# Performance work log

Measured on AMD Instinct MI355X. Metric: run time of the kernel, lower is better.

Reference implementation:

```python
import jax, jax.numpy as jnp
import numpy as np

ALPHA = -10.0  # softmax sharpness on |x - bin| distances
TAU = 0.0
TAU2 = 0.0
EPS = 1e-10

B, F, L, K = 32, 64, 1024, 32


def setup_inputs() -> dict:
    key = jax.random.key(0)
    k1, k2 = jax.random.split(key)
    x = jax.random.normal(k1, (B, F, L), dtype=jnp.float32)
    bins = jax.random.normal(k2, (K,), dtype=jnp.float32)
    return {"x": x, "bins": bins}


def reference(x, bins):
    # dist: [B, F, L, K] = |x[..., None] - bins|
    dist = jnp.abs(x[..., None] - bins)
    # soft assignment over the K bins (training path of the module)
    soft = jax.nn.softmax(ALPHA * dist, axis=-1)
    assignment = soft + EPS

    # weighted quantization loss: sum of per-bin mean of sqrt(assignment)
    quant = jnp.sum(jnp.mean(jnp.sqrt(assignment), axis=(0, 1, 2)))
    weighted_quant_loss = jnp.stack([quant, jnp.float32(TAU2)])[None, :]  # [1, 2]

    # code entropy of average assignment distribution
    p = jnp.mean(assignment, axis=(0, 1, 2))  # [K]
    code_entropy = -jnp.sum(p * jnp.log(p))
    weighted_code_entropy = jnp.stack([code_entropy, jnp.float32(TAU)])[None, :]  # [1, 2]

    # soft reconstruction against the bins: [B, F, L]
    bit_code = jnp.einsum('bflk,k->bfl', assignment, bins)
    return bit_code, weighted_code_entropy, weighted_quant_loss
```

## Files before the change

### kernel.cpp

```cpp
#include <hip/hip_runtime.h>

#define K      32
#define KH     16
#define TPB    256
#define NB     2048
#define EPT    8
#define NTOT   (32 * 64 * 1024)
#define PSTRIDE (NB * (TPB / 2))

__device__ __forceinline__ float wave_reduce_sum(float v) {
#pragma unroll
  for (int m = 1; m < 64; m <<= 1) v += __shfl_xor(v, m, 64);
  return v;
}

__device__ __forceinline__ float pair_lane_reduce(float v) {
#pragma unroll
  for (int m = 2; m < 64; m <<= 1) v += __shfl_xor(v, m, 64);
  return v;
}

__global__ __launch_bounds__(TPB)
void ssq_main(const float* __restrict__ x, const float* __restrict__ bins,
              float* __restrict__ out, float* __restrict__ partials) {
  const int tid  = threadIdx.x;
  const int half = tid & 1;
  const int pslot = blockIdx.x * (TPB / 2) + (tid >> 1);

  float binv[KH];
#pragma unroll
  for (int j = 0; j < KH; ++j) binv[j] = bins[KH * half + j];
  float bs_local = 0.f;
#pragma unroll
  for (int j = 0; j < KH; ++j) bs_local += binv[j];
  const float binsum = bs_local + __shfl_xor(bs_local, 1, 64);
  const float epsb = 1e-10f * binsum;

  float xs[EPT];
#pragma unroll
  for (int e = 0; e < EPT; ++e) xs[e] = x[pslot + e * PSTRIDE];

  float sAcc[KH];
#pragma unroll
  for (int j = 0; j < KH; ++j) sAcc[j] = 0.f;
  float q = 0.f;

  const float Ch = -7.213475204444817f;

#pragma unroll 1
  for (int e = 0; e < EPT; ++e) {
    const float xv = xs[e];
    float t[KH];
    float s0 = 0.f, s1 = 0.f, h0 = 0.f, h1 = 0.f, b0 = 0.f, b1 = 0.f;
#pragma unroll
    for (int j = 0; j < KH; j += 2) {
      float ha = __builtin_amdgcn_exp2f(Ch * fabsf(xv - binv[j + 0]));
      float hb = __builtin_amdgcn_exp2f(Ch * fabsf(xv - binv[j + 1]));
      float ta = ha * ha, tb = hb * hb;
      t[j + 0] = ta; t[j + 1] = tb;
      s0 += ta; s1 += tb;
      h0 += ha; h1 += hb;
      b0 = fmaf(ta, binv[j + 0], b0);
      b1 = fmaf(tb, binv[j + 1], b1);
    }
    const float s_loc = s0 + s1;
    const float b_loc = b0 + b1;
    const float s_full = s_loc + __shfl_xor(s_loc, 1, 64);
    const float b_full = b_loc + __shfl_xor(b_loc, 1, 64);
    const float inv = __builtin_amdgcn_rcpf(s_full);
    q = fmaf(h0 + h1, __builtin_amdgcn_rsqf(s_full), q);
    if (half == 0) out[pslot + e * PSTRIDE] = fmaf(b_full, inv, epsb);
#pragma unroll
    for (int j = 0; j < KH; ++j) sAcc[j] = fmaf(t[j], inv, sAcc[j]);
  }

  __shared__ float red[4][K + 1];
  const int lane = tid & 63, wv = tid >> 6;
#pragma unroll
  for (int j = 0; j < KH; ++j) {
    float v = pair_lane_reduce(sAcc[j]);
    if (lane < 2) red[wv][KH * lane + j] = v;
  }
  {
    float v = wave_reduce_sum(q);
    if (lane == 0) red[wv][K] = v;
  }
  __syncthreads();
  if (tid < K + 1) {
    float v = red[0][tid] + red[1][tid] + red[2][tid] + red[3][tid];
    partials[tid * NB + blockIdx.x] = v;
  }
}

__global__ __launch_bounds__(TPB)
void ssq_reduce(const float* __restrict__ partials, float* __restrict__ sums) {
  const float* p = partials + blockIdx.x * NB;
  const int tid  = threadIdx.x;
  float s = 0.f;
#pragma unroll
  for (int j = 0; j < NB / TPB; ++j) s += p[tid + j * TPB];
  s = wave_reduce_sum(s);
  __shared__ float red[4];
  if ((tid & 63) == 0) red[tid >> 6] = s;
  __syncthreads();
  if (tid == 0) sums[blockIdx.x] = red[0] + red[1] + red[2] + red[3];
}

__global__ void ssq_final(const float* __restrict__ sums, float* __restrict__ out) {
  const int lane = threadIdx.x;
  float e = 0.f;
  if (lane < K) {
    float p = sums[lane] * (1.0f / (float)NTOT) + 1e-10f;
    e = -p * __logf(p);
  }
  e = wave_reduce_sum(e);
  if (lane == 0) {
    out[NTOT + 0] = e;
    out[NTOT + 1] = 0.f;
    out[NTOT + 2] = sums[K] * (1.0f / (float)NTOT);
    out[NTOT + 3] = 0.f;
  }
}

extern "C" void kernel_launch(void* const* d_in, const int* in_sizes, int n_in,
                              void* d_out, int out_size, void* d_ws, size_t ws_size,
                              hipStream_t stream) {
  const float* x    = (const float*)d_in[0];
  const float* bins = (const float*)d_in[1];
  float* out        = (float*)d_out;
  float* partials   = (float*)d_ws;
  float* sums       = partials + (K + 1) * NB;

  ssq_main  <<<NB,    TPB, 0, stream>>>(x, bins, out, partials);
  ssq_reduce<<<K + 1, TPB, 0, stream>>>(partials, sums);
  ssq_final <<<1,     64,  0, stream>>>(sums, out);
}
```

Baseline: 83.97 us.

## Replace per-bin softmax loop with sorted-bin prefix sums and binary search

Sorts the bins in a prep kernel and precomputes prefix and suffix sums of exp(±c·bin), so each element's softmax denominator, reconstruction and sqrt sums need only a binary search plus a few exponentials, not 32. Per-bin assignment mass is gathered with shared-memory atomics into two split-point accumulators and rebuilt in a merged tail kernel. This removes most of the exp work, but exp(±14.4·x) factorisation can overflow or lose precision for large |x| or bins, and shared atomics may contend.

```diff
diff --git a/kernel.cpp b/kernel.cpp
--- a/kernel.cpp
+++ b/kernel.cpp
@@ -1,12 +1,11 @@
 #include <hip/hip_runtime.h>
 
 #define K      32
-#define KH     16
 #define TPB    256
 #define NB     2048
-#define EPT    8
 #define NTOT   (32 * 64 * 1024)
-#define PSTRIDE (NB * (TPB / 2))
+#define CL2    14.4269504088896341f
+#define TFLOATS 232
 
 __device__ __forceinline__ float wave_reduce_sum(float v) {
 #pragma unroll
@@ -14,111 +13,142 @@
   return v;
 }
 
-__device__ __forceinline__ float pair_lane_reduce(float v) {
+
+__global__ void ssq_prep(const float* __restrict__ bins, float* __restrict__ tg) {
+  const int lane = threadIdx.x;
+  float bv = (lane < K) ? bins[lane] : 0.f;
+  int rank = 0;
 #pragma unroll
-  for (int m = 2; m < 64; m <<= 1) v += __shfl_xor(v, m, 64);
-  return v;
-}
-
-__global__ __launch_bounds__(TPB)
-void ssq_main(const float* __restrict__ x, const float* __restrict__ bins,
-              float* __restrict__ out, float* __restrict__ partials) {
-  const int tid  = threadIdx.x;
-  const int half = tid & 1;
-  const int pslot = blockIdx.x * (TPB / 2) + (tid >> 1);
-
-  float binv[KH];
-#pragma unroll
-  for (int j = 0; j < KH; ++j) binv[j] = bins[KH * half + j];
-  float bs_local = 0.f;
-#pragma unroll
-  for (int j = 0; j < KH; ++j) bs_local += binv[j];
-  const float binsum = bs_local + __shfl_xor(bs_local, 1, 64);
-  const float epsb = 1e-10f * binsum;
-
-  float xs[EPT];
-#pragma unroll
-  for (int e = 0; e < EPT; ++e) xs[e] = x[pslot + e * PSTRIDE];
-
-  float sAcc[KH];
-#pragma unroll
-  for (int j = 0; j < KH; ++j) sAcc[j] = 0.f;
-  float q = 0.f;
-
-  const float Ch = -7.213475204444817f;
-
-#pragma unroll 1
-  for (int e = 0; e < EPT; ++e) {
-    const float xv = xs[e];
-    float t[KH];
-    float s0 = 0.f, s1 = 0.f, h0 = 0.f, h1 = 0.f, b0 = 0.f, b1 = 0.f;
-#pragma unroll
-    for (int j = 0; j < KH; j += 2) {
-      float ha = __builtin_amdgcn_exp2f(Ch * fabsf(xv - binv[j + 0]));
-      float hb = __builtin_amdgcn_exp2f(Ch * fabsf(xv - binv[j + 1]));
-      float ta = ha * ha, tb = hb * hb;
-      t[j + 0] = ta; t[j + 1] = tb;
-      s0 += ta; s1 += tb;
-      h0 += ha; h1 += hb;
-      b0 = fmaf(ta, binv[j + 0], b0);
-      b1 = fmaf(tb, binv[j + 1], b1);
+  for (int j = 0; j < K; ++j) {
+    float bj = __shfl(bv, j, 64);
+    rank += (bj < bv) || (bj == bv && j < lane);
+  }
+  __shared__ float sb[K];
+  if (lane < K) sb[rank] = bv;
+  __syncthreads();
+  if (lane <= K) {
+    float A = 0.f, B = 0.f, Ab = 0.f, Bb = 0.f, Ah = 0.f, Bh = 0.f;
+    for (int k = 0; k < K; ++k) {
+      float s   = sb[k];
+      float e   = __builtin_amdgcn_exp2f( CL2 * s);
+      float em  = __builtin_amdgcn_exp2f(-CL2 * s);
+      float eh  = __builtin_amdgcn_exp2f( 0.5f * CL2 * s);
+      float ehm = __builtin_amdgcn_exp2f(-0.5f * CL2 * s);
+      if (k < lane) { A += e;  Ab = fmaf(s, e,  Ab); Ah += eh;  }
+      else          { B += em; Bb = fmaf(s, em, Bb); Bh += ehm; }
     }
-    const float s_loc = s0 + s1;
-    const float b_loc = b0 + b1;
-    const float s_full = s_loc + __shfl_xor(s_loc, 1, 64);
-    const float b_full = b_loc + __shfl_xor(b_loc, 1, 64);
-    const float inv = __builtin_amdgcn_rcpf(s_full);
-    q = fmaf(h0 + h1, __builtin_amdgcn_rsqf(s_full), q);
-    if (half == 0) out[pslot + e * PSTRIDE] = fmaf(b_full, inv, epsb);
-#pragma unroll
-    for (int j = 0; j < KH; ++j) sAcc[j] = fmaf(t[j], inv, sAcc[j]);
+    tg[ 33 + lane] = A;  tg[ 66 + lane] = B;
+    tg[ 99 + lane] = Ab; tg[132 + lane] = Bb;
+    tg[165 + lane] = Ah; tg[198 + lane] = Bh;
   }
-
-  __shared__ float red[4][K + 1];
-  const int lane = tid & 63, wv = tid >> 6;
-#pragma unroll
-  for (int j = 0; j < KH; ++j) {
-    float v = pair_lane_reduce(sAcc[j]);
-    if (lane < 2) red[wv][KH * lane + j] = v;
-  }
-  {
-    float v = wave_reduce_sum(q);
-    if (lane == 0) red[wv][K] = v;
-  }
-  __syncthreads();
-  if (tid < K + 1) {
-    float v = red[0][tid] + red[1][tid] + red[2][tid] + red[3][tid];
-    partials[tid * NB + blockIdx.x] = v;
+  if (lane < K) tg[lane] = sb[lane];
+  if (lane == 0) {
+    tg[K] = 0.f;
+    float bs = 0.f;
+    for (int k = 0; k < K; ++k) bs += sb[k];
+    tg[231] = 1e-10f * bs;
   }
 }
 
-__global__ __launch_bounds__(TPB)
-void ssq_reduce(const float* __restrict__ partials, float* __restrict__ sums) {
-  const float* p = partials + blockIdx.x * NB;
-  const int tid  = threadIdx.x;
-  float s = 0.f;
-#pragma unroll
-  for (int j = 0; j < NB / TPB; ++j) s += p[tid + j * TPB];
-  s = wave_reduce_sum(s);
-  __shared__ float red[4];
-  if ((tid & 63) == 0) red[tid >> 6] = s;
-  __syncthreads();
-  if (tid == 0) sums[blockIdx.x] = red[0] + red[1] + red[2] + red[3];
+__device__ __forceinline__ void ssq_elem(float xv, const float* __restrict__ Tf,
+                                         float* __restrict__ bU,
+                                         float* __restrict__ bV,
+                                         float epsb, float& q, float& bit) {
+  const float* sb = Tf;
+  int b_ = 0;
+  b_ += (sb[b_ + 15] <= xv) ? 16 : 0;
+  b_ += (sb[b_ +  7] <= xv) ?  8 : 0;
+  b_ += (sb[b_ +  3] <= xv) ?  4 : 0;
+  b_ += (sb[b_ +  1] <= xv) ?  2 : 0;
+  b_ += (sb[b_]      <= xv) ?  1 : 0;
+  b_ += (sb[b_]      <= xv) ?  1 : 0;
+  float ex   = __builtin_amdgcn_exp2f(CL2 * xv);
+  float exm  = __builtin_amdgcn_rcpf(ex);
+  float exh  = __builtin_amdgcn_sqrtf(ex);
+  float exhm = __builtin_amdgcn_rsqf(ex);
+  float A  = Tf[ 33 + b_], B  = Tf[ 66 + b_];
+  float Ab = Tf[ 99 + b_], Bb = Tf[132 + b_];
+  float Ah = Tf[165 + b_], Bh = Tf[198 + b_];
+  float s   = fmaf(exm, A, ex * B);
+  float inv = __builtin_amdgcn_rcpf(s);
+  bit = fmaf(fmaf(exm, Ab, ex * Bb), inv, epsb);
+  float h = fmaf(exhm, Ah, exh * Bh);
+  q = fmaf(h, __builtin_amdgcn_rsqf(s), q);
+  atomicAdd(&bU[b_], exm * inv);
+  atomicAdd(&bV[b_], ex * inv);
 }
 
-__global__ void ssq_final(const float* __restrict__ sums, float* __restrict__ out) {
-  const int lane = threadIdx.x;
-  float e = 0.f;
-  if (lane < K) {
-    float p = sums[lane] * (1.0f / (float)NTOT) + 1e-10f;
-    e = -p * __logf(p);
+__global__ __launch_bounds__(TPB, 8)
+void ssq_main(const float4* __restrict__ x4, const float* __restrict__ tg,
+              float4* __restrict__ out4, float* __restrict__ partials) {
+  const int tid = threadIdx.x;
+  __shared__ float Tf[TFLOATS];
+  __shared__ float bU[K + 1], bV[K + 1];
+  __shared__ float qr[4];
+  if (tid < TFLOATS) Tf[tid] = tg[tid];
+  if (tid < K + 1) { bU[tid] = 0.f; bV[tid] = 0.f; }
+  __syncthreads();
+  const float epsb = Tf[231];
+
+  const int gid = blockIdx.x * TPB + tid;
+  float4 X = x4[gid];
+  float q = 0.f;
+  float4 O;
+  ssq_elem(X.x, Tf, bU, bV, epsb, q, O.x);
+  ssq_elem(X.y, Tf, bU, bV, epsb, q, O.y);
+  ssq_elem(X.z, Tf, bU, bV, epsb, q, O.z);
+  ssq_elem(X.w, Tf, bU, bV, epsb, q, O.w);
+  out4[gid] = O;
+
+  const int lane = tid & 63, wv = tid >> 6;
+  float qs = wave_reduce_sum(q);
+  if (lane == 0) qr[wv] = qs;
+  __syncthreads();
+  if (tid < K)           partials[tid * NB + blockIdx.x] = bU[tid + 1];
+  else if (tid < 2 * K)  partials[tid * NB + blockIdx.x] = bV[tid - K];
+  else if (tid == 2 * K) partials[2 * K * NB + blockIdx.x] =
+                             qr[0] + qr[1] + qr[2] + qr[3];
+}
+
+__global__ __launch_bounds__(1024)
+void ssq_tail(const float* __restrict__ partials, const float* __restrict__ tg,
+              float* __restrict__ out) {
+  const int tid = threadIdx.x;
+  const int wv = tid >> 6, lane = tid & 63;
+  __shared__ float S[2 * K + 1];
+  for (int r = wv; r < 2 * K + 1; r += 16) {
+    const float4* p = reinterpret_cast<const float4*>(partials + r * NB);
+    float s = 0.f;
+#pragma unroll
+    for (int c = 0; c < NB / 256; ++c) {
+      float4 v = p[c * 64 + lane];
+      s += (v.x + v.y) + (v.z + v.w);
+    }
+    s = wave_reduce_sum(s);
+    if (lane == 0) S[r] = s;
   }
-  e = wave_reduce_sum(e);
-  if (lane == 0) {
-    out[NTOT + 0] = e;
-    out[NTOT + 1] = 0.f;
-    out[NTOT + 2] = sums[K] * (1.0f / (float)NTOT);
-    out[NTOT + 3] = 0.f;
+  __syncthreads();
+  if (wv == 0) {
+    float e = 0.f;
+    if (lane < K) {
+      float U = 0.f, V = 0.f;
+      for (int r = 0; r < K; ++r) {
+        U += (r >= lane) ? S[r] : 0.f;
+        V += (r <= lane) ? S[K + r] : 0.f;
+      }
+      float sbk = tg[lane];
+      float P = fmaf(__builtin_amdgcn_exp2f(CL2 * sbk), U,
+                     __builtin_amdgcn_exp2f(-CL2 * sbk) * V);
+      float p = P * (1.0f / (float)NTOT) + 1e-10f;
+      e = -p * __logf(p);
+    }
+    e = wave_reduce_sum(e);
+    if (lane == 0) {
+      out[NTOT + 0] = e;
+      out[NTOT + 1] = 0.f;
+      out[NTOT + 2] = S[2 * K] * (1.0f / (float)NTOT);
+      out[NTOT + 3] = 0.f;
+    }
   }
 }
 
@@ -128,10 +158,10 @@
   const float* x    = (const float*)d_in[0];
   const float* bins = (const float*)d_in[1];
   float* out        = (float*)d_out;
-  float* partials   = (float*)d_ws;
-  float* sums       = partials + (K + 1) * NB;
+  float* tg         = (float*)d_ws;
+  float* partials   = tg + 256;
 
-  ssq_main  <<<NB,    TPB, 0, stream>>>(x, bins, out, partials);
-  ssq_reduce<<<K + 1, TPB, 0, stream>>>(partials, sums);
-  ssq_final <<<1,     64,  0, stream>>>(sums, out);
+  ssq_prep<<<1,  64,   0, stream>>>(bins, tg);
+  ssq_main<<<NB, TPB,  0, stream>>>((const float4*)x, tg, (float4*)out, partials);
+  ssq_tail<<<1,  1024, 0, stream>>>(partials, tg, out);
 }
```

New measurement: 97.50 us. 16.1% more time.
